# Optimization experiments

Hardware: AMD Instinct MI355X
Metric: run time of the kernel (lower is better)

## Reference

```python
import jax, jax.numpy as jnp
import numpy as np

EPS = 1e-12  # F.normalize default eps

def _l2norm(x, axis):
    n = jnp.sqrt(jnp.sum(x * x, axis=axis, keepdims=True))
    return x / jnp.maximum(n, EPS)

def setup_inputs() -> dict:
    key = jax.random.key(0)
    k1, k2 = jax.random.split(key)
    B, S, H, L = 64, 1024, 1024, 3
    deep_features = jax.random.normal(k1, (B, S, H), dtype=jnp.float32)
    label_embeddings = jax.random.normal(k2, (H, L), dtype=jnp.float32)
    attention_mask = jnp.ones((B, S), dtype=jnp.float32)
    return {"deep_features": deep_features,
            "label_embeddings": label_embeddings,
            "attention_mask": attention_mask}

def reference(deep_features, label_embeddings, attention_mask):
    # L2-normalize features over hidden dim, labels over hidden (dim=0)
    df_n = _l2norm(deep_features, axis=-1)              # [B,S,H]
    le_n = _l2norm(label_embeddings, axis=0)            # [H,L]
    atten = jnp.einsum('bsh,hl->bsl', df_n, le_n)       # [B,S,L]
    # additive mask bias: 10000*(mask-1), broadcast over L
    bias = 10000.0 * (attention_mask - 1.0)             # [B,S]
    atten = atten + bias[:, :, None]                    # [B,S,L]
    # MaxPool1d(kernel=3, stride=3) over L; L==3 -> single window, then squeeze
    pooled = jnp.max(atten, axis=-1)                    # [B,S]
    normalized = jax.nn.softmax(pooled, axis=1)         # softmax over seq dim
    # weighted sum of features: [B,1,S] @ [B,S,H] -> [B,H]
    feature_attention = jnp.einsum('bs,bsh->bh', normalized, deep_features)
    return (feature_attention, atten, normalized[:, None, :])
```

## Files before the change

kernel.cpp:

```cpp
#include <hip/hip_runtime.h>
#include <math.h>

constexpr int B = 64;
constexpr int S = 1024;
constexpr int H = 1024;
constexpr int L = 3;
#define NEPS 1e-12f

__device__ __forceinline__ float wave_reduce_sum(float v) {
    #pragma unroll
    for (int off = 32; off > 0; off >>= 1) v += __shfl_xor(v, off);
    return v;
}
__device__ __forceinline__ float wave_reduce_max(float v) {
    #pragma unroll
    for (int off = 32; off > 0; off >>= 1) v = fmaxf(v, __shfl_xor(v, off));
    return v;
}

__global__ __launch_bounds__(256) void norm_labels(const float* __restrict__ le,
                                                   float* __restrict__ leT) {
    __shared__ float red[L][4];
    __shared__ float rn[L];
    const int tid = threadIdx.x;
    const int wid = tid >> 6, lane = tid & 63;

    float acc[L] = {0.f, 0.f, 0.f};
    for (int h = tid; h < H; h += 256) {
        #pragma unroll
        for (int l = 0; l < L; ++l) {
            float v = le[h * L + l];
            acc[l] += v * v;
        }
    }
    #pragma unroll
    for (int l = 0; l < L; ++l) {
        float s = wave_reduce_sum(acc[l]);
        if (lane == 0) red[l][wid] = s;
    }
    __syncthreads();
    if (tid < L) {
        float s = red[tid][0] + red[tid][1] + red[tid][2] + red[tid][3];
        rn[tid] = 1.0f / fmaxf(sqrtf(s), NEPS);
    }
    __syncthreads();
    for (int h = tid; h < H; h += 256) {
        #pragma unroll
        for (int l = 0; l < L; ++l)
            leT[l * H + h] = le[h * L + l] * rn[l];
    }
}

__global__ __launch_bounds__(256) void row_kernel(const float* __restrict__ df,
                                                  const float* __restrict__ leT,
                                                  const float* __restrict__ mask,
                                                  float* __restrict__ atten) {
    const int row = blockIdx.x;
    const int tid = threadIdx.x;
    const int wid = tid >> 6, lane = tid & 63;

    const float4 d  = *(const float4*)(df  + (size_t)row * H + tid * 4);
    const float4 l0 = *(const float4*)(leT + 0 * H + tid * 4);
    const float4 l1 = *(const float4*)(leT + 1 * H + tid * 4);
    const float4 l2 = *(const float4*)(leT + 2 * H + tid * 4);

    float ssq = d.x * d.x + d.y * d.y + d.z * d.z + d.w * d.w;
    float d0  = d.x * l0.x + d.y * l0.y + d.z * l0.z + d.w * l0.w;
    float d1  = d.x * l1.x + d.y * l1.y + d.z * l1.z + d.w * l1.w;
    float d2  = d.x * l2.x + d.y * l2.y + d.z * l2.z + d.w * l2.w;

    __shared__ float red[4][4];
    ssq = wave_reduce_sum(ssq);
    d0  = wave_reduce_sum(d0);
    d1  = wave_reduce_sum(d1);
    d2  = wave_reduce_sum(d2);
    if (lane == 0) {
        red[0][wid] = ssq; red[1][wid] = d0; red[2][wid] = d1; red[3][wid] = d2;
    }
    __syncthreads();
    if (tid == 0) {
        float tssq = red[0][0] + red[0][1] + red[0][2] + red[0][3];
        float td0  = red[1][0] + red[1][1] + red[1][2] + red[1][3];
        float td1  = red[2][0] + red[2][1] + red[2][2] + red[2][3];
        float td2  = red[3][0] + red[3][1] + red[3][2] + red[3][3];
        float rnrm = 1.0f / fmaxf(sqrtf(tssq), NEPS);
        float bias = 10000.0f * (mask[row] - 1.0f);
        float* o = atten + (size_t)row * L;
        o[0] = td0 * rnrm + bias;
        o[1] = td1 * rnrm + bias;
        o[2] = td2 * rnrm + bias;
    }
}

__global__ __launch_bounds__(256) void softmax_kernel(const float* __restrict__ atten,
                                                      float* __restrict__ norm) {
    const int b = blockIdx.x;
    const int tid = threadIdx.x;
    const int wid = tid >> 6, lane = tid & 63;

    float p[4];
    float m = -INFINITY;
    #pragma unroll
    for (int i = 0; i < 4; ++i) {
        int s = i * 256 + tid;
        const float* a = atten + ((size_t)b * S + s) * L;
        p[i] = fmaxf(fmaxf(a[0], a[1]), a[2]);
        m = fmaxf(m, p[i]);
    }
    __shared__ float redm[4];
    __shared__ float reds[4];
    __shared__ float bm, bsum;
    m = wave_reduce_max(m);
    if (lane == 0) redm[wid] = m;
    __syncthreads();
    if (tid == 0)
        bm = fmaxf(fmaxf(redm[0], redm[1]), fmaxf(redm[2], redm[3]));
    __syncthreads();
    float mm = bm;
    float e[4], ssum = 0.f;
    #pragma unroll
    for (int i = 0; i < 4; ++i) {
        e[i] = expf(p[i] - mm);
        ssum += e[i];
    }
    ssum = wave_reduce_sum(ssum);
    if (lane == 0) reds[wid] = ssum;
    __syncthreads();
    if (tid == 0) bsum = reds[0] + reds[1] + reds[2] + reds[3];
    __syncthreads();
    float rs = 1.0f / bsum;
    #pragma unroll
    for (int i = 0; i < 4; ++i) {
        int s = i * 256 + tid;
        norm[(size_t)b * S + s] = e[i] * rs;
    }
}

constexpr int SCHUNK = 64;
__global__ __launch_bounds__(256) void weighted_sum(const float* __restrict__ df,
                                                    const float* __restrict__ norm,
                                                    float* __restrict__ fa) {
    const int c = blockIdx.x;
    const int b = blockIdx.y;
    const int tid = threadIdx.x;

    __shared__ float w[SCHUNK];
    if (tid < SCHUNK) w[tid] = norm[(size_t)b * S + c * SCHUNK + tid];
    __syncthreads();

    const float* base = df + ((size_t)b * S + (size_t)c * SCHUNK) * H + tid * 4;
    float4 acc = make_float4(0.f, 0.f, 0.f, 0.f);
    #pragma unroll 4
    for (int i = 0; i < SCHUNK; ++i) {
        float4 d = *(const float4*)(base + (size_t)i * H);
        float ww = w[i];
        acc.x += ww * d.x;
        acc.y += ww * d.y;
        acc.z += ww * d.z;
        acc.w += ww * d.w;
    }
    float* o = fa + (size_t)b * H + tid * 4;
    atomicAdd(o + 0, acc.x);
    atomicAdd(o + 1, acc.y);
    atomicAdd(o + 2, acc.z);
    atomicAdd(o + 3, acc.w);
}

extern "C" void kernel_launch(void* const* d_in, const int* in_sizes, int n_in,
                              void* d_out, int out_size, void* d_ws, size_t ws_size,
                              hipStream_t stream) {
    const float* df   = (const float*)d_in[0];
    const float* le   = (const float*)d_in[1];
    const float* mask = (const float*)d_in[2];

    float* out   = (float*)d_out;
    float* fa    = out;
    float* atten = out + (size_t)B * H;
    float* norm  = atten + (size_t)B * S * L;

    float* leT = (float*)d_ws;

    hipMemsetAsync(fa, 0, (size_t)B * H * sizeof(float), stream);

    norm_labels<<<1, 256, 0, stream>>>(le, leT);
    row_kernel<<<B * S, 256, 0, stream>>>(df, leT, mask, atten);
    softmax_kernel<<<B, 256, 0, stream>>>(atten, norm);
    weighted_sum<<<dim3(S / SCHUNK, B), 256, 0, stream>>>(df, norm, fa);
}
```

Measured before the change: 395.9 us.

## Process one row per wave, emit pooled values, fold memset into softmax

The row kernel now gives each wave a whole row, so each block handles four rows. This removes the cross-wave shared-memory reduction and the block barrier, and cuts the block count by four. The row kernel also writes the per-row max to a workspace buffer, so softmax reads one contiguous vector with float4 loads. Softmax now zeroes the output accumulator, which replaces the separate memset. The weighted-sum chunk is halved and its unroll deepened, which doubles the number of blocks and atomics.

```diff
diff --git a/kernel.cpp b/kernel.cpp
--- a/kernel.cpp
+++ b/kernel.cpp
@@ -54,89 +54,79 @@
 __global__ __launch_bounds__(256) void row_kernel(const float* __restrict__ df,
                                                   const float* __restrict__ leT,
                                                   const float* __restrict__ mask,
-                                                  float* __restrict__ atten) {
-    const int row = blockIdx.x;
-    const int tid = threadIdx.x;
-    const int wid = tid >> 6, lane = tid & 63;
+                                                  float* __restrict__ atten,
+                                                  float* __restrict__ pooled) {
+    const int wid = threadIdx.x >> 6, lane = threadIdx.x & 63;
+    const int row = blockIdx.x * 4 + wid;
+    const float* r = df + (size_t)row * H;
 
-    const float4 d  = *(const float4*)(df  + (size_t)row * H + tid * 4);
-    const float4 l0 = *(const float4*)(leT + 0 * H + tid * 4);
-    const float4 l1 = *(const float4*)(leT + 1 * H + tid * 4);
-    const float4 l2 = *(const float4*)(leT + 2 * H + tid * 4);
-
-    float ssq = d.x * d.x + d.y * d.y + d.z * d.z + d.w * d.w;
-    float d0  = d.x * l0.x + d.y * l0.y + d.z * l0.z + d.w * l0.w;
-    float d1  = d.x * l1.x + d.y * l1.y + d.z * l1.z + d.w * l1.w;
-    float d2  = d.x * l2.x + d.y * l2.y + d.z * l2.z + d.w * l2.w;
-
-    __shared__ float red[4][4];
-    ssq = wave_reduce_sum(ssq);
-    d0  = wave_reduce_sum(d0);
-    d1  = wave_reduce_sum(d1);
-    d2  = wave_reduce_sum(d2);
+    float ssq = 0.f, d0 = 0.f, d1 = 0.f, d2 = 0.f;
+    #pragma unroll
+    for (int k = 0; k < 4; ++k) {
+        const int idx = (k * 64 + lane) * 4;
+        const float4 d  = *(const float4*)(r + idx);
+        const float4 a0 = *(const float4*)(leT + 0 * H + idx);
+        const float4 a1 = *(const float4*)(leT + 1 * H + idx);
+        const float4 a2 = *(const float4*)(leT + 2 * H + idx);
+        ssq += d.x * d.x  + d.y * d.y  + d.z * d.z  + d.w * d.w;
+        d0  += d.x * a0.x + d.y * a0.y + d.z * a0.z + d.w * a0.w;
+        d1  += d.x * a1.x + d.y * a1.y + d.z * a1.z + d.w * a1.w;
+        d2  += d.x * a2.x + d.y * a2.y + d.z * a2.z + d.w * a2.w;
+    }
+    #pragma unroll
+    for (int off = 32; off > 0; off >>= 1) {
+        ssq += __shfl_xor(ssq, off);
+        d0  += __shfl_xor(d0, off);
+        d1  += __shfl_xor(d1, off);
+        d2  += __shfl_xor(d2, off);
+    }
     if (lane == 0) {
-        red[0][wid] = ssq; red[1][wid] = d0; red[2][wid] = d1; red[3][wid] = d2;
-    }
-    __syncthreads();
-    if (tid == 0) {
-        float tssq = red[0][0] + red[0][1] + red[0][2] + red[0][3];
-        float td0  = red[1][0] + red[1][1] + red[1][2] + red[1][3];
-        float td1  = red[2][0] + red[2][1] + red[2][2] + red[2][3];
-        float td2  = red[3][0] + red[3][1] + red[3][2] + red[3][3];
-        float rnrm = 1.0f / fmaxf(sqrtf(tssq), NEPS);
-        float bias = 10000.0f * (mask[row] - 1.0f);
+        const float rnrm = 1.0f / fmaxf(sqrtf(ssq), NEPS);
+        const float bias = 10000.0f * (mask[row] - 1.0f);
+        const float v0 = d0 * rnrm + bias;
+        const float v1 = d1 * rnrm + bias;
+        const float v2 = d2 * rnrm + bias;
         float* o = atten + (size_t)row * L;
-        o[0] = td0 * rnrm + bias;
-        o[1] = td1 * rnrm + bias;
-        o[2] = td2 * rnrm + bias;
+        o[0] = v0; o[1] = v1; o[2] = v2;
+        pooled[row] = fmaxf(fmaxf(v0, v1), v2);
     }
 }
 
-__global__ __launch_bounds__(256) void softmax_kernel(const float* __restrict__ atten,
-                                                      float* __restrict__ norm) {
+__global__ __launch_bounds__(256) void softmax_kernel(const float* __restrict__ pooled,
+                                                      float* __restrict__ norm,
+                                                      float* __restrict__ fa) {
     const int b = blockIdx.x;
     const int tid = threadIdx.x;
     const int wid = tid >> 6, lane = tid & 63;
 
-    float p[4];
-    float m = -INFINITY;
-    #pragma unroll
-    for (int i = 0; i < 4; ++i) {
-        int s = i * 256 + tid;
-        const float* a = atten + ((size_t)b * S + s) * L;
-        p[i] = fmaxf(fmaxf(a[0], a[1]), a[2]);
-        m = fmaxf(m, p[i]);
-    }
+    *(float4*)(fa + (size_t)b * H + tid * 4) = make_float4(0.f, 0.f, 0.f, 0.f);
+
+    const float4 p = *(const float4*)(pooled + (size_t)b * S + tid * 4);
+
     __shared__ float redm[4];
     __shared__ float reds[4];
-    __shared__ float bm, bsum;
+    float m = fmaxf(fmaxf(p.x, p.y), fmaxf(p.z, p.w));
     m = wave_reduce_max(m);
     if (lane == 0) redm[wid] = m;
     __syncthreads();
-    if (tid == 0)
-        bm = fmaxf(fmaxf(redm[0], redm[1]), fmaxf(redm[2], redm[3]));
-    __syncthreads();
-    float mm = bm;
-    float e[4], ssum = 0.f;
-    #pragma unroll
-    for (int i = 0; i < 4; ++i) {
-        e[i] = expf(p[i] - mm);
-        ssum += e[i];
-    }
+    m = fmaxf(fmaxf(redm[0], redm[1]), fmaxf(redm[2], redm[3]));
+
+    float4 e;
+    e.x = expf(p.x - m);
+    e.y = expf(p.y - m);
+    e.z = expf(p.z - m);
+    e.w = expf(p.w - m);
+    float ssum = e.x + e.y + e.z + e.w;
     ssum = wave_reduce_sum(ssum);
     if (lane == 0) reds[wid] = ssum;
     __syncthreads();
-    if (tid == 0) bsum = reds[0] + reds[1] + reds[2] + reds[3];
-    __syncthreads();
-    float rs = 1.0f / bsum;
-    #pragma unroll
-    for (int i = 0; i < 4; ++i) {
-        int s = i * 256 + tid;
-        norm[(size_t)b * S + s] = e[i] * rs;
-    }
+    const float rs = 1.0f / (reds[0] + reds[1] + reds[2] + reds[3]);
+
+    e.x *= rs; e.y *= rs; e.z *= rs; e.w *= rs;
+    *(float4*)(norm + (size_t)b * S + tid * 4) = e;
 }
 
-constexpr int SCHUNK = 64;
+constexpr int SCHUNK = 32;
 __global__ __launch_bounds__(256) void weighted_sum(const float* __restrict__ df,
                                                     const float* __restrict__ norm,
                                                     float* __restrict__ fa) {
@@ -150,10 +140,10 @@
 
     const float* base = df + ((size_t)b * S + (size_t)c * SCHUNK) * H + tid * 4;
     float4 acc = make_float4(0.f, 0.f, 0.f, 0.f);
-    #pragma unroll 4
+    #pragma unroll 8
     for (int i = 0; i < SCHUNK; ++i) {
-        float4 d = *(const float4*)(base + (size_t)i * H);
-        float ww = w[i];
+        const float4 d = *(const float4*)(base + (size_t)i * H);
+        const float ww = w[i];
         acc.x += ww * d.x;
         acc.y += ww * d.y;
         acc.z += ww * d.z;
@@ -178,12 +168,11 @@
     float* atten = out + (size_t)B * H;
     float* norm  = atten + (size_t)B * S * L;
 
-    float* leT = (float*)d_ws;
-
-    hipMemsetAsync(fa, 0, (size_t)B * H * sizeof(float), stream);
+    float* leT    = (float*)d_ws;
+    float* pooled = leT + (size_t)L * H;
 
     norm_labels<<<1, 256, 0, stream>>>(le, leT);
-    row_kernel<<<B * S, 256, 0, stream>>>(df, leT, mask, atten);
-    softmax_kernel<<<B, 256, 0, stream>>>(atten, norm);
+    row_kernel<<<(B * S) / 4, 256, 0, stream>>>(df, leT, mask, atten, pooled);
+    softmax_kernel<<<B, 256, 0, stream>>>(pooled, norm, fa);
     weighted_sum<<<dim3(S / SCHUNK, B), 256, 0, stream>>>(df, norm, fa);
 }
```

Measured after the change: 403.8 us. About the same (+2.0%).
